# Optimization experiments

Measured on AMD Instinct MI355X. Metric: run time of the kernel, lower is better.

The kernel has to match this reference:

```python
import jax, jax.numpy as jnp
import numpy as np

EPS = 1e-12
SMOOTH = 9.0
SGR_STEPS = 3


def l2norm(x, axis=-1):
    return x / jnp.maximum(jnp.linalg.norm(x, axis=axis, keepdims=True), EPS)


def setup_inputs() -> dict:
    key = jax.random.key(0)
    d, s = 1024, 256
    n_img, n_cap, L, n_tok = 64, 64, 32, 197  # 197 -> CLS + 14x14 grid

    def xavier(k, shape):
        lim = float(np.sqrt(6.0 / (shape[-2] + shape[-1])))
        return jax.random.uniform(k, shape, jnp.float32, -lim, lim)

    ks = iter(jax.random.split(key, 32))
    inp = {
        "img_embs": jax.random.normal(next(ks), (n_img, n_tok, d), jnp.float32),
        "cap_embs": jax.random.normal(next(ks), (n_cap, L, d), jnp.float32),
        # constant lengths == max length so the vectorized reference matches
        # the original per-caption loop exactly
        "cap_lens": jnp.full((n_cap,), L, dtype=jnp.int32),
        # visual GlobalSelfAttention
        "vG_Wl": xavier(next(ks), (d, d)), "vG_bl": jnp.zeros((d,), jnp.float32),
        "vG_Wg": xavier(next(ks), (d, d)), "vG_bg": jnp.zeros((d,), jnp.float32),
        "vG_Wc": xavier(next(ks), (d, 1)), "vG_bc": jnp.zeros((1,), jnp.float32),
        # textual GlobalSelfAttention
        "tG_Wl": xavier(next(ks), (d, d)), "tG_bl": jnp.zeros((d,), jnp.float32),
        "tG_Wg": xavier(next(ks), (d, d)), "tG_bg": jnp.zeros((d,), jnp.float32),
        "tG_Wc": xavier(next(ks), (d, 1)), "tG_bc": jnp.zeros((1,), jnp.float32),
        # similarity projections
        "W_loc": xavier(next(ks), (d, s)), "b_loc": jnp.zeros((s,), jnp.float32),
        "W_glo": xavier(next(ks), (d, s)), "b_glo": jnp.zeros((s,), jnp.float32),
        "W_eval": xavier(next(ks), (s, 1)), "b_eval": jnp.zeros((1,), jnp.float32),
        # 3 stacked GraphReasoning layers
        "sgr_Wq": xavier(next(ks), (SGR_STEPS, s, s)), "sgr_bq": jnp.zeros((SGR_STEPS, s), jnp.float32),
        "sgr_Wk": xavier(next(ks), (SGR_STEPS, s, s)), "sgr_bk": jnp.zeros((SGR_STEPS, s), jnp.float32),
        "sgr_Wg": xavier(next(ks), (SGR_STEPS, s, s)), "sgr_bg": jnp.zeros((SGR_STEPS, s), jnp.float32),
    }
    return inp


def global_self_attention(local, raw_global, Wl, bl, Wg, bg, Wc, bc):
    # local: (B, N, d), raw_global: (B, d); dropout is identity at eval
    le = jnp.tanh(local @ Wl + bl)
    ge = jnp.tanh(raw_global @ Wg + bg)
    logits = ((le * ge[:, None, :]) @ Wc + bc)[..., 0]  # (B, N)
    weights = jax.nn.softmax(logits, axis=1)
    global_feat = jnp.sum(weights[..., None] * local, axis=1)
    return l2norm(global_feat, axis=-1)


def scan_attention(query, context, smooth=SMOOTH):
    # query: (B, Nq, d), context: (B, Nc, d)
    attn = jnp.einsum("bcd,bqd->bcq", context, query)
    attn = jax.nn.leaky_relu(attn, negative_slope=0.1)
    attn = l2norm(attn, axis=2)                    # normalize over query dim
    attn = jnp.swapaxes(attn, 1, 2)                # (B, Nq, Nc)
    attn = jax.nn.softmax(attn * smooth, axis=2)   # softmax over context
    weighted = jnp.einsum("bqc,bcd->bqd", attn, context)
    return l2norm(weighted, axis=-1)


def graph_reasoning(sim_emb, Wq, bq, Wk, bk, Wg, bg):
    q = sim_emb @ Wq + bq
    k = sim_emb @ Wk + bk
    edge = jax.nn.softmax(jnp.einsum("bnd,bmd->bnm", q, k), axis=-1)
    sgr = jnp.einsum("bnm,bmd->bnd", edge, sim_emb)
    return jax.nn.relu(sgr @ Wg + bg)


def reference(img_embs, cap_embs, cap_lens,
              vG_Wl, vG_bl, vG_Wg, vG_bg, vG_Wc, vG_bc,
              tG_Wl, tG_bl, tG_Wg, tG_bg, tG_Wc, tG_bc,
              W_loc, b_loc, W_glo, b_glo, W_eval, b_eval,
              sgr_Wq, sgr_bq, sgr_Wk, sgr_bk, sgr_Wg, sgr_bg):
    # 197 tokens -> strip CLS (has_cls_token is True)
    img_tokens = img_embs[:, 1:, :]                      # (n_img, 196, d)
    n_img = img_tokens.shape[0]
    img_avg = img_tokens.mean(axis=1)
    img_global = global_self_attention(img_tokens, img_avg,
                                       vG_Wl, vG_bl, vG_Wg, vG_bg, vG_Wc, vG_bc)

    def per_caption(cap_i):                              # cap_i: (L, d)
        L, d = cap_i.shape
        cap_e = jnp.broadcast_to(cap_i[None], (n_img, L, d))
        cap_avg = jnp.broadcast_to(cap_i.mean(axis=0)[None], (n_img, d))
        cap_global = global_self_attention(cap_e, cap_avg,
                                           tG_Wl, tG_bl, tG_Wg, tG_bg, tG_Wc, tG_bc)
        ctx = scan_attention(cap_e, img_tokens)          # (n_img, L, d)
        sim_loc = l2norm((ctx - cap_e) ** 2 @ W_loc + b_loc, axis=-1)
        sim_glo = l2norm((img_global - cap_global) ** 2 @ W_glo + b_glo, axis=-1)
        sim_emb = jnp.concatenate([sim_glo[:, None, :], sim_loc], axis=1)
        for t in range(SGR_STEPS):
            sim_emb = graph_reasoning(sim_emb, sgr_Wq[t], sgr_bq[t],
                                      sgr_Wk[t], sgr_bk[t], sgr_Wg[t], sgr_bg[t])
        return jax.nn.sigmoid(sim_emb[:, 0, :] @ W_eval + b_eval)[:, 0]  # (n_img,)

    sims = jax.vmap(per_caption)(cap_embs)               # (n_cap, n_img)
    return sims.T                                        # (n_img, n_cap)
```

## Files before the change

kernel.cpp:

```cpp
#include <hip/hip_runtime.h>
#include <hip/hip_bf16.h>
#include <math.h>

#define NI 64
#define NC 64
#define NTOK 197
#define TT 196
#define CL 32
#define DD 1024
#define SS 256
#define NN 33
#define EPSN 1e-12f
#define SMOOTHF 9.0f
#define TP 224

typedef __attribute__((ext_vector_type(8))) short bfrag;
typedef __attribute__((ext_vector_type(4))) float f32x4;
#define MFMA(a, b, c) __builtin_amdgcn_mfma_f32_16x16x32_bf16((a), (b), (c), 0, 0, 0)

#define OFF_ATTNT  0
#define OFF_WTILE  14848
#define OFF_WMAX   23552
#define OFF_NRMS   24064
#define OFF_QN     24192
#define OFF_RNQ    24704
#define OFF_SEA    0
#define OFF_EB     17424
#define OFF_R1     22176
#define OFF_WKQ    29088
#define OFF_VBUF   30112
#define SMEM_BYTES 31392

__device__ __forceinline__ float warp_reduce_sum64(float v) {
#pragma unroll
  for (int m = 32; m > 0; m >>= 1) v += __shfl_xor(v, m, 64);
  return v;
}
__device__ __forceinline__ unsigned short f2b(float f) {
  __hip_bfloat16 h = __float2bfloat16(f);
  return *reinterpret_cast<unsigned short*>(&h);
}
__device__ __forceinline__ float b2f(unsigned short u) {
  union { unsigned int i; float f; } v;
  v.i = ((unsigned int)u) << 16;
  return v.f;
}

__global__ void k_avg(const float* __restrict__ img, const float* __restrict__ cap,
                      float* __restrict__ img_avg, float* __restrict__ cap_avg) {
  int bid = blockIdx.x;
  int tid = threadIdx.x;
  if (bid < NI) {
    int b = bid;
    for (int d = tid; d < DD; d += 256) {
      float acc = 0.f;
      const float* p = img + ((size_t)b * NTOK + 1) * DD + d;
      for (int t = 0; t < TT; ++t) acc += p[(size_t)t * DD];
      img_avg[b * DD + d] = acc * (1.0f / TT);
    }
  } else {
    int c = bid - NI;
    for (int d = tid; d < DD; d += 256) {
      float acc = 0.f;
      const float* p = cap + (size_t)c * CL * DD + d;
      for (int t = 0; t < CL; ++t) acc += p[(size_t)t * DD];
      cap_avg[c * DD + d] = acc * (1.0f / CL);
    }
  }
}

__global__ void k_hvec2(const float* __restrict__ img_avg, const float* __restrict__ cap_avg,
                        const float* __restrict__ vWg, const float* __restrict__ vbg,
                        const float* __restrict__ vWc, const float* __restrict__ tWg,
                        const float* __restrict__ tbg, const float* __restrict__ tWc,
                        float* __restrict__ h_img, float* __restrict__ h_cap) {
  __shared__ float av[DD];
  int bid = blockIdx.x;
  const float* avg;
  const float* Wg;
  const float* bg;
  const float* Wc;
  float* h;
  if (bid < 256) {
    avg = img_avg; Wg = vWg; bg = vbg; Wc = vWc; h = h_img;
  } else {
    avg = cap_avg; Wg = tWg; bg = tbg; Wc = tWc; h = h_cap; bid -= 256;
  }
  int b = bid >> 2;
  int dc = bid & 3;
  int tid = threadIdx.x;
  for (int i = tid; i < DD; i += 256) av[i] = avg[b * DD + i];
  __syncthreads();
  int d = dc * 256 + tid;
  float acc = 0.f;
  for (int k = 0; k < DD; k += 4) {
    float4 a4 = *(const float4*)&av[k];
    acc += a4.x * Wg[(size_t)(k + 0) * DD + d];
    acc += a4.y * Wg[(size_t)(k + 1) * DD + d];
    acc += a4.z * Wg[(size_t)(k + 2) * DD + d];
    acc += a4.w * Wg[(size_t)(k + 3) * DD + d];
  }
  h[b * DD + d] = tanhf(acc + bg[d]) * Wc[d];
}

__global__ void k_logits2(const unsigned short* __restrict__ Ai, const unsigned short* __restrict__ Wi,
                          const float* __restrict__ bli, const float* __restrict__ hi,
                          float* __restrict__ pi,
                          const unsigned short* __restrict__ Ac, const unsigned short* __restrict__ Wc2,
                          const float* __restrict__ blc, const float* __restrict__ hc,
                          float* __restrict__ pc) {
  int tid = threadIdx.x;
  int lane = tid & 63, w = tid >> 6;
  int lrow = lane & 15, lk = (lane >> 4) * 8, rsub = (lane >> 4) * 4;
  int bx = blockIdx.x;
  const unsigned short* Abf;
  const unsigned short* WT;
  const float* bl;
  const float* h;
  float* partial;
  int rb, rowsPerBatch;
  if (bx < 196) {
    Abf = Ai; WT = Wi; bl = bli; h = hi; partial = pi; rb = bx * 64; rowsPerBatch = TT;
  } else {
    Abf = Ac; WT = Wc2; bl = blc; h = hc; partial = pc; rb = (bx - 196) * 64; rowsPerBatch = CL;
  }
  int c0 = blockIdx.y * 64;
  const unsigned short* ap = Abf + (size_t)(rb + w * 16 + lrow) * DD;
  f32x4 acc[4] = {};
  for (int k0 = 0; k0 < DD; k0 += 32) {
    bfrag a = *(const bfrag*)(ap + k0 + lk);
#pragma unroll
    for (int i = 0; i < 4; ++i) {
      bfrag bb = *(const bfrag*)(WT + (size_t)(c0 + i * 16 + lrow) * DD + k0 + lk);
      acc[i] = MFMA(a, bb, acc[i]);
    }
  }
#pragma unroll
  for (int r = 0; r < 4; ++r) {
    int row = rb + w * 16 + rsub + r;
    int bb2 = row / rowsPerBatch;
    float s = 0.f;
#pragma unroll
    for (int i = 0; i < 4; ++i) {
      int col = c0 + i * 16 + lrow;
      s += tanhf(acc[i][r] + bl[col]) * h[bb2 * DD + col];
    }
    s += __shfl_xor(s, 1, 64);
    s += __shfl_xor(s, 2, 64);
    s += __shfl_xor(s, 4, 64);
    s += __shfl_xor(s, 8, 64);
    if (lrow == 0) partial[(size_t)row * 16 + blockIdx.y] = s;
  }
}

__global__ void k_finish2(const float* __restrict__ pi, const float* __restrict__ bci,
                          const float* __restrict__ Xi, long bsi, int Ri, float* __restrict__ oi,
                          const float* __restrict__ pc, const float* __restrict__ bcc,
                          const float* __restrict__ Xc, long bsc, int Rc, float* __restrict__ oc) {
  __shared__ float w[200];
  __shared__ float red[8];
  int bid = blockIdx.x, tid = threadIdx.x;
  const float* partial;
  const float* bc;
  const float* Xbase;
  long batchStride;
  int R, b;
  float* outG;
  if (bid < 64) {
    partial = pi; bc = bci; Xbase = Xi; batchStride = bsi; R = Ri; outG = oi; b = bid;
  } else {
    partial = pc; bc = bcc; Xbase = Xc; batchStride = bsc; R = Rc; outG = oc; b = bid - 64;
  }
  for (int t = tid; t < R; t += 256) {
    const float* pp = &partial[((size_t)b * R + t) * 16];
    float s = bc[0];
#pragma unroll
    for (int u = 0; u < 16; ++u) s += pp[u];
    w[t] = s;
  }
  __syncthreads();
  float m = -1e30f;
  for (int t = tid; t < R; t += 256) m = fmaxf(m, w[t]);
#pragma unroll
  for (int mm = 32; mm; mm >>= 1) m = fmaxf(m, __shfl_xor(m, mm, 64));
  if ((tid & 63) == 0) red[tid >> 6] = m;
// ... 1 lines not shown
  m = fmaxf(fmaxf(red[0], red[1]), fmaxf(red[2], red[3]));
  __syncthreads();
  for (int t = tid; t < R; t += 256) w[t] = expf(w[t] - m);
  __syncthreads();
  const float* xb = Xbase + (size_t)b * batchStride;
  float acc[4];
  float ss = 0.f;
#pragma unroll
  for (int c4 = 0; c4 < 4; ++c4) {
    int d = tid + c4 * 256;
    float a = 0.f;
    for (int t = 0; t < R; ++t) a += w[t] * xb[(size_t)t * DD + d];
    acc[c4] = a;
    ss += a * a;
  }
  ss = warp_reduce_sum64(ss);
  if ((tid & 63) == 0) red[tid >> 6] = ss;
  __syncthreads();
  ss = red[0] + red[1] + red[2] + red[3];
  float rn = 1.0f / fmaxf(sqrtf(ss), EPSN);
#pragma unroll
  for (int c4 = 0; c4 < 4; ++c4) outG[(size_t)b * DD + tid + c4 * 256] = acc[c4] * rn;
}

__global__ void k_simglo_m(const float* __restrict__ ig, const float* __restrict__ cg,
                           const unsigned short* __restrict__ wgloT,
                           const float* __restrict__ bgl, float* __restrict__ simglo) {
  __shared__ unsigned short aL[64 * 40];
  int tid = threadIdx.x;
  int lane = tid & 63, w = tid >> 6;
  int lrow = lane & 15, lk = (lane >> 4) * 8, rsub = (lane >> 4) * 4;
  int b = blockIdx.x;
  int srow = tid >> 2, skq = tid & 3;
  f32x4 acc[16] = {};
  for (int k0 = 0; k0 < DD; k0 += 32) {
    const float* ip = ig + (size_t)b * DD + k0 + skq * 8;
    const float* cp = cg + (size_t)srow * DD + k0 + skq * 8;
    float4 i0 = *(const float4*)ip;
    float4 i1 = *(const float4*)(ip + 4);
    float4 c0 = *(const float4*)cp;
    float4 c1 = *(const float4*)(cp + 4);
    float d0 = i0.x - c0.x, d1 = i0.y - c0.y, d2 = i0.z - c0.z, d3 = i0.w - c0.w;
    float d4 = i1.x - c1.x, d5 = i1.y - c1.y, d6 = i1.z - c1.z, d7 = i1.w - c1.w;
    uint4 o;
    o.x = (unsigned int)f2b(d0 * d0) | ((unsigned int)f2b(d1 * d1) << 16);
    o.y = (unsigned int)f2b(d2 * d2) | ((unsigned int)f2b(d3 * d3) << 16);
    o.z = (unsigned int)f2b(d4 * d4) | ((unsigned int)f2b(d5 * d5) << 16);
    o.w = (unsigned int)f2b(d6 * d6) | ((unsigned int)f2b(d7 * d7) << 16);
    __syncthreads();
    *(uint4*)&aL[srow * 40 + skq * 8] = o;
    __syncthreads();
    bfrag af = *(const bfrag*)&aL[(w * 16 + lrow) * 40 + lk];
#pragma unroll
    for (int ct = 0; ct < 16; ++ct) {
      bfrag bb = *(const bfrag*)(wgloT + (size_t)(ct * 16 + lrow) * DD + k0 + lk);
      acc[ct] = MFMA(af, bb, acc[ct]);
    }
  }
  float bglv[16];
#pragma unroll
  for (int ct = 0; ct < 16; ++ct) bglv[ct] = bgl[ct * 16 + lrow];
#pragma unroll
  for (int r = 0; r < 4; ++r) {
    int crow = w * 16 + rsub + r;
    float vv[16];
    float ssq = 0.f;
#pragma unroll
    for (int ct = 0; ct < 16; ++ct) {
      float v = acc[ct][r] + bglv[ct];
      vv[ct] = v;
      ssq += v * v;
    }
    ssq += __shfl_xor(ssq, 1, 64);
    ssq += __shfl_xor(ssq, 2, 64);
    ssq += __shfl_xor(ssq, 4, 64);
    ssq += __shfl_xor(ssq, 8, 64);
    float rn = 1.0f / fmaxf(sqrtf(ssq), EPSN);
    float* op = simglo + ((size_t)b * 64 + crow) * SS;
#pragma unroll
    for (int ct = 0; ct < 16; ++ct) op[ct * 16 + lrow] = vv[ct] * rn;
  }
}

__global__ void k_mmatb(const float* __restrict__ Wa, const float* __restrict__ Wb,
                        unsigned short* __restrict__ M, const float* __restrict__ bq,
                        float* __restrict__ wkbqv) {
  __shared__ float a_lds[32][68];
  __shared__ float b_lds[32][68];
  __shared__ float bv[SS];
  int tid = threadIdx.x;
  if (blockIdx.x >= 48) {
    int t = blockIdx.x - 48;
    const float* wk = Wb + (size_t)t * SS * SS;
    bv[tid] = bq[t * SS + tid];
    __syncthreads();
    float acc = 0.f;
    for (int j = 0; j < SS; j += 4) {
      float4 wv = *(const float4*)&wk[(size_t)tid * SS + j];
      float4 b4 = *(const float4*)&bv[j];
      acc += wv.x * b4.x + wv.y * b4.y + wv.z * b4.z + wv.w * b4.w;
    }
    wkbqv[t * SS + tid] = acc;
    return;
  }
  int t = blockIdx.x >> 4;
  int dt = (blockIdx.x >> 2) & 3, et = blockIdx.x & 3;
  int d0 = dt * 64, e0 = et * 64;
  const float* wq = Wa + (size_t)t * SS * SS;
  const float* wk = Wb + (size_t)t * SS * SS;
  int ty = tid >> 4, tx = tid & 15;
  int s_rr = tid >> 2, s_kq = tid & 3;
  float acc[4][4] = {};
  for (int j0 = 0; j0 < SS; j0 += 32) {
    float4 q0 = *(const float4*)&wq[(size_t)(d0 + s_rr) * SS + j0 + s_kq * 8];
    float4 q1 = *(const float4*)&wq[(size_t)(d0 + s_rr) * SS + j0 + s_kq * 8 + 4];
    float4 k0v = *(const float4*)&wk[(size_t)(e0 + s_rr) * SS + j0 + s_kq * 8];
    float4 k1v = *(const float4*)&wk[(size_t)(e0 + s_rr) * SS + j0 + s_kq * 8 + 4];
    __syncthreads();
    float qa[8] = {q0.x, q0.y, q0.z, q0.w, q1.x, q1.y, q1.z, q1.w};
    float ka[8] = {k0v.x, k0v.y, k0v.z, k0v.w, k1v.x, k1v.y, k1v.z, k1v.w};
#pragma unroll
    for (int u = 0; u < 8; ++u) {
      a_lds[s_kq * 8 + u][s_rr] = qa[u];
      b_lds[s_kq * 8 + u][s_rr] = ka[u];
    }
    __syncthreads();
#pragma unroll
    for (int kk = 0; kk < 32; ++kk) {
      float4 a4 = *(const float4*)&a_lds[kk][ty * 4];
      float4 b4 = *(const float4*)&b_lds[kk][tx * 4];
      float av[4] = {a4.x, a4.y, a4.z, a4.w};
      float bvv[4] = {b4.x, b4.y, b4.z, b4.w};
#pragma unroll
      for (int i = 0; i < 4; ++i)
#pragma unroll
        for (int j = 0; j < 4; ++j) acc[i][j] += av[i] * bvv[j];
    }
  }
#pragma unroll
  for (int i = 0; i < 4; ++i) {
    unsigned int lo = (unsigned int)f2b(acc[i][0]) | ((unsigned int)f2b(acc[i][1]) << 16);
    unsigned int hi = (unsigned int)f2b(acc[i][2]) | ((unsigned int)f2b(acc[i][3]) << 16);
    uint2 o = make_uint2(lo, hi);
    *(uint2*)(M + (size_t)t * SS * SS + (size_t)(d0 + ty * 4 + i) * SS + e0 + tx * 4) = o;
  }
}

__global__ void k_imgprep(const float* __restrict__ img, unsigned short* __restrict__ row_bf,
                          unsigned short* __restrict__ tr_bf) {
  __shared__ float t[32][33];
  int b = blockIdx.z;
  int t0 = blockIdx.y * 32, d0 = blockIdx.x * 32;
  int tx = threadIdx.x & 31, ty = threadIdx.x >> 5;
#pragma unroll
  for (int u = 0; u < 4; ++u) {
    int tt = t0 + ty + u * 8;
    float v = (tt < TT) ? img[((size_t)b * NTOK + 1 + tt) * DD + d0 + tx] : 0.f;
    t[ty + u * 8][tx] = v;
    if (tt < TT) row_bf[((size_t)b * TT + tt) * DD + d0 + tx] = f2b(v);
  }
  __syncthreads();
#pragma unroll
  for (int u = 0; u < 4; ++u)
    tr_bf[((size_t)b * DD + d0 + ty + u * 8) * TP + t0 + tx] = f2b(t[tx][ty + u * 8]);
}

__global__ void k_gram_mfma(const unsigned short* __restrict__ img_bf,
                            unsigned short* __restrict__ gram) {
  int tid = threadIdx.x;
  int lane = tid & 63, w = tid >> 6;
  int lrow = lane & 15, lk = (lane >> 4) * 8, rsub = (lane >> 4) * 4;
  int bimg = blockIdx.x;
  int rb = blockIdx.y * 64, cb = blockIdx.z * 64;
  const unsigned short* X = img_bf + (size_t)bimg * TT * DD;
  int ra = rb + w * 16 + lrow;
  if (ra > TT - 1) ra = TT - 1;
  f32x4 acc[4] = {};
  for (int k0 = 0; k0 < DD; k0 += 32) {
    bfrag a = *(const bfrag*)(X + (size_t)ra * DD + k0 + lk);
#pragma unroll
    for (int i = 0; i < 4; ++i) {
      int cc = cb + i * 16 + lrow;
      if (cc > TT - 1) cc = TT - 1;
      bfrag bb = *(const bfrag*)(X + (size_t)cc * DD + k0 + lk);
      acc[i] = MFMA(a, bb, acc[i]);
    }
  }
  unsigned short* Gp = gram + (size_t)bimg * 208 * TP;
#pragma unroll
  for (int i = 0; i < 4; ++i) {
    int cc = cb + i * 16 + lrow;
#pragma unroll
    for (int r = 0; r < 4; ++r) {
      int rr = rb + w * 16 + rsub + r;
      if (rr < 208 && cc < TP)
        Gp[(size_t)rr * TP + cc] = (rr < TT && cc < TT) ? f2b(acc[i][r]) : 0;
    }
  }
}

__global__ void k_castb(const float* __restrict__ s, unsigned short* __restrict__ d, int n4) {
  int i = blockIdx.x * 256 + threadIdx.x;
  if (i < n4) {
    float4 v = *(const float4*)(s + (size_t)i * 4);
    uint2 o;
    o.x = (unsigned int)f2b(v.x) | ((unsigned int)f2b(v.y) << 16);
    o.y = (unsigned int)f2b(v.z) | ((unsigned int)f2b(v.w) << 16);
    *(uint2*)(d + (size_t)i * 4) = o;
  }
}

__global__ void k_tcast_all(const float* __restrict__ vWl, const float* __restrict__ tWl,
                            const float* __restrict__ sWg, const float* __restrict__ Wloc,
                            const float* __restrict__ Wglo,
                            unsigned short* __restrict__ wlT_v, unsigned short* __restrict__ wlT_t,
                            unsigned short* __restrict__ wgT3, unsigned short* __restrict__ wlocT,
                            unsigned short* __restrict__ wgloT) {
  __shared__ float t[32][33];
  int id = blockIdx.x;
  const float* s;
  unsigned short* d;
  int R, C;
  if (id < 1024) {
    s = vWl; d = wlT_v; R = 1024; C = 1024;
  } else if (id < 2048) {
    s = tWl; d = wlT_t; R = 1024; C = 1024; id -= 1024;
  } else if (id < 2240) {
    id -= 2048;
    int tb = id >> 6; id &= 63;
    s = sWg + (size_t)tb * 65536; d = wgT3 + (size_t)tb * 65536; R = 256; C = 256;
  } else if (id < 2496) {
    s = Wloc; d = wlocT; R = 1024; C = 256; id -= 2240;
  } else {
    s = Wglo; d = wgloT; R = 1024; C = 256; id -= 2496;
  }
  int ct = C >> 5;
  int r0 = (id / ct) * 32, c0 = (id % ct) * 32;
  int tx = threadIdx.x & 31, ty = threadIdx.x >> 5;
#pragma unroll
  for (int u = 0; u < 4; ++u)
    t[ty + u * 8][tx] = s[(size_t)(r0 + ty + u * 8) * C + c0 + tx];
  __syncthreads();
#pragma unroll
  for (int u = 0; u < 4; ++u)
    d[(size_t)(c0 + ty + u * 8) * R + r0 + tx] = f2b(t[tx][ty + u * 8]);
}

__global__ __launch_bounds__(256, 4) void k_pair(
    const float* __restrict__ b_loc, const float* __restrict__ simglo,
    const float* __restrict__ wkbq, const float* __restrict__ bg3,
    const float* __restrict__ W_eval, const float* __restrict__ b_eval,
    const unsigned short* __restrict__ cap_bf, const unsigned short* __restrict__ img_bf,
    const unsigned short* __restrict__ imgT_bf, const unsigned short* __restrict__ gram_bf,
    const unsigned short* __restrict__ wlocT_bf, const unsigned short* __restrict__ mt_bf,
    const unsigned short* __restrict__ wgT_bf, float* __restrict__ out) {
  extern __shared__ char smem[];

  int tid = threadIdx.x;
  int lane = tid & 63, w = tid >> 6;
  int lrow = lane & 15;
  int lk = (lane >> 4) * 8;
  int rsub = (lane >> 4) * 4;
  int p = ((blockIdx.x & 7) << 9) | (blockIdx.x >> 3);
  int b = p >> 6, c = p & 63;
  const unsigned short* imgR = img_bf + (size_t)b * TT * DD;
  const unsigned short* capB = cap_bf + (size_t)c * CL * DD;
  char* attnT_b = smem + OFF_ATTNT;

  {
    f32x4 acc[4][2] = {};
    for (int k0 = 0; k0 < DD; k0 += 32) {
      bfrag bq0 = *(const bfrag*)(capB + (size_t)lrow * DD + k0 + lk);
      bfrag bq1 = *(const bfrag*)(capB + (size_t)(16 + lrow) * DD + k0 + lk);
#pragma unroll
      for (int i = 0; i < 4; ++i) {
        int tt = w + 4 * i;
        if (tt < 13) {
          int t = tt * 16 + lrow;
          bfrag a = {0, 0, 0, 0, 0, 0, 0, 0};
          if (t < TT) a = *(const bfrag*)(imgR + (size_t)t * DD + k0 + lk);
          acc[i][0] = MFMA(a, bq0, acc[i][0]);
          acc[i][1] = MFMA(a, bq1, acc[i][1]);
        }
      }
    }
    float mx0 = -1e30f, mx1 = -1e30f;
#pragma unroll
    for (int i = 0; i < 4; ++i) {
      int tt = w + 4 * i;
      if (tt < 13) {
#pragma unroll
        for (int r = 0; r < 4; ++r) {
          int t = tt * 16 + rsub + r;
          float v0 = acc[i][0][r];
          v0 = v0 < 0.f ? 0.1f * v0 : v0;
          float v1 = acc[i][1][r];
          v1 = v1 < 0.f ? 0.1f * v1 : v1;
          float s2 = v0 * v0 + v1 * v1;
          s2 += __shfl_xor(s2, 1, 64);
          s2 += __shfl_xor(s2, 2, 64);
          s2 += __shfl_xor(s2, 4, 64);
          s2 += __shfl_xor(s2, 8, 64);
          float rn = 1.0f / fmaxf(sqrtf(s2), EPSN);
          v0 *= rn;
          v1 *= rn;
          acc[i][0][r] = v0;
          acc[i][1][r] = v1;
          if (t < TT) {
            mx0 = fmaxf(mx0, v0);
            mx1 = fmaxf(mx1, v1);
          }
        }
      }
    }
    mx0 = fmaxf(mx0, __shfl_xor(mx0, 16, 64));
    mx0 = fmaxf(mx0, __shfl_xor(mx0, 32, 64));
    mx1 = fmaxf(mx1, __shfl_xor(mx1, 16, 64));
    mx1 = fmaxf(mx1, __shfl_xor(mx1, 32, 64));
    float* wmax = (float*)(smem + OFF_WMAX);
    if ((lane >> 4) == 0) {
      wmax[w * 32 + lrow] = mx0;
      wmax[w * 32 + 16 + lrow] = mx1;
    }
    __syncthreads();
    mx0 = fmaxf(fmaxf(wmax[lrow], wmax[32 + lrow]), fmaxf(wmax[64 + lrow], wmax[96 + lrow]));
    mx1 = fmaxf(fmaxf(wmax[16 + lrow], wmax[48 + lrow]),
                fmaxf(wmax[80 + lrow], wmax[112 + lrow]));
#pragma unroll
    for (int i = 0; i < 4; ++i) {
      int tt = w + 4 * i;
// ... 177 lines not shown
      const unsigned short* mstep = mt_bf + (size_t)step * SS * SS;
      const unsigned short* wstep = wgT_bf + (size_t)step * SS * SS;
      wkq[tid] = wkbq[step * SS + tid];
      __syncthreads();
      if (tid < 132) {
        int m = tid >> 2, qq = tid & 3;
        float a = 0.f;
        for (int e = qq * 64; e < qq * 64 + 64; e += 2) {
          unsigned int u = *(const unsigned int*)(seA_b + m * 528 + e * 2);
          a += b2f(u & 0xffff) * wkq[e] + b2f(u >> 16) * wkq[e + 1];
        }
        a += __shfl_xor(a, 1, 64);
        a += __shfl_xor(a, 2, 64);
        if (qq == 0) vbuf[m] = a;
      }
      f32x4 aE[3] = {};
      for (int ec = 0; ec < 4; ++ec) {
        f32x4 aGc[3] = {};
        for (int kc = 0; kc < 8; ++kc) {
          int k = kc * 32 + lk;
          bfrag bb = *(const bfrag*)(mstep + (size_t)(ec * 64 + w * 16 + lrow) * SS + k);
#pragma unroll
          for (int mt = 0; mt < 3; ++mt) {
            bfrag af = *(const bfrag*)(seA_b + (mt * 16 + lrow) * 528 + k * 2);
            aGc[mt] = MFMA(af, bb, aGc[mt]);
          }
        }
        __syncthreads();
#pragma unroll
        for (int mt = 0; mt < 3; ++mt)
#pragma unroll
          for (int r = 0; r < 4; ++r)
            *(unsigned short*)(Gc_b + (mt * 16 + rsub + r) * 144 + (w * 16 + lrow) * 2) =
                f2b(aGc[mt][r]);
        __syncthreads();
#pragma unroll
        for (int kc = 0; kc < 2; ++kc) {
          int k = kc * 32 + lk;
#pragma unroll
          for (int ti = 0; ti < 3; ++ti) {
            int tile = w + ti * 4;
            if (tile < 9) {
              int mtE = tile / 3, ntE = tile - mtE * 3;
              bfrag ga = *(const bfrag*)(Gc_b + (mtE * 16 + lrow) * 144 + k * 2);
              bfrag sb = *(const bfrag*)(seA_b + (ntE * 16 + lrow) * 528 + (ec * 64 + k) * 2);
              aE[ti] = MFMA(ga, sb, aE[ti]);
            }
          }
        }
      }
      __syncthreads();
#pragma unroll
      for (int ti = 0; ti < 3; ++ti) {
        int tile = w + ti * 4;
        if (tile < 9) {
          int mtE = tile / 3, ntE = tile - mtE * 3;
          int n0 = mtE * 16 + rsub, m = ntE * 16 + lrow;
#pragma unroll
          for (int r = 0; r < 4; ++r)
            if (n0 + r < NN && m < NN) Ef[(n0 + r) * 34 + m] = aE[ti][r] + vbuf[m];
        }
      }
      __syncthreads();
      if (tid < NN) {
        float mx = -1e30f;
        for (int mm = 0; mm < NN; ++mm) mx = fmaxf(mx, Ef[tid * 34 + mm]);
        float sum = 0.f;
        for (int mm = 0; mm < NN; ++mm) {
          float e = expf(Ef[tid * 34 + mm] - mx);
          Ef[tid * 34 + mm] = e;
          sum += e;
        }
        float rs = 1.0f / sum;
        for (int mm = 0; mm < NN; ++mm) Ef[tid * 34 + mm] *= rs;
      }
      __syncthreads();
      for (int idx = tid; idx < 33 * 36; idx += 256) {
        int n = idx / 36, mp = (idx - n * 36) * 2;
        unsigned int lo = (mp < NN) ? (unsigned int)f2b(Ef[n * 34 + mp]) : 0u;
        unsigned int hi = (mp + 1 < NN) ? (unsigned int)f2b(Ef[n * 34 + mp + 1]) : 0u;
        *(unsigned int*)(Eb + n * 144 + mp * 2) = lo | (hi << 16);
      }
      __syncthreads();
      unsigned int oPk[4][3][2];
#pragma unroll
      for (int sc = 0; sc < 4; ++sc) {
        f32x4 aX[3] = {};
        for (int kc = 0; kc < 8; ++kc) {
          int k = kc * 32 + lk;
          bfrag bb = *(const bfrag*)(wstep + (size_t)(sc * 64 + w * 16 + lrow) * SS + k);
#pragma unroll
          for (int mt = 0; mt < 3; ++mt) {
            bfrag af = *(const bfrag*)(seA_b + (mt * 16 + lrow) * 528 + k * 2);
            aX[mt] = MFMA(af, bb, aX[mt]);
          }
        }
        __syncthreads();
#pragma unroll
        for (int mt = 0; mt < 3; ++mt) {
          unsigned int lo = (unsigned int)f2b(aX[mt][0]) | ((unsigned int)f2b(aX[mt][1]) << 16);
          unsigned int hi = (unsigned int)f2b(aX[mt][2]) | ((unsigned int)f2b(aX[mt][3]) << 16);
          *(uint2*)(XT_b + (w * 16 + lrow) * 144 + (mt * 16 + rsub) * 2) = make_uint2(lo, hi);
        }
        *(uint2*)(XT_b + (w * 16 + lrow) * 144 + (48 + rsub) * 2) = make_uint2(0, 0);
        __syncthreads();
        f32x4 aO[3] = {};
#pragma unroll
        for (int kc = 0; kc < 2; ++kc) {
          int k = kc * 32 + lk;
          bfrag xa = *(const bfrag*)(XT_b + (w * 16 + lrow) * 144 + k * 2);
#pragma unroll
          for (int nt = 0; nt < 3; ++nt) {
            bfrag eb = *(const bfrag*)(Eb + (nt * 16 + lrow) * 144 + k * 2);
            aO[nt] = MFMA(xa, eb, aO[nt]);
          }
        }
        float bga[4];
#pragma unroll
        for (int r = 0; r < 4; ++r) bga[r] = bg3[step * SS + sc * 64 + w * 16 + rsub + r];
#pragma unroll
        for (int nt = 0; nt < 3; ++nt) {
          float v0 = fmaxf(aO[nt][0] + bga[0], 0.f);
          float v1 = fmaxf(aO[nt][1] + bga[1], 0.f);
          float v2 = fmaxf(aO[nt][2] + bga[2], 0.f);
          float v3 = fmaxf(aO[nt][3] + bga[3], 0.f);
          oPk[sc][nt][0] = (unsigned int)f2b(v0) | ((unsigned int)f2b(v1) << 16);
          oPk[sc][nt][1] = (unsigned int)f2b(v2) | ((unsigned int)f2b(v3) << 16);
        }
      }
#pragma unroll
      for (int sc = 0; sc < 4; ++sc)
#pragma unroll
        for (int nt = 0; nt < 3; ++nt) {
          int n = nt * 16 + lrow;
          if (n < NN)
            *(uint2*)(seA_b + n * 528 + (sc * 64 + w * 16 + rsub) * 2) =
                make_uint2(oPk[sc][nt][0], oPk[sc][nt][1]);
        }
      __syncthreads();
    }
  }

  if (tid < 64) {
    const char* seA_b = smem + OFF_SEA;
    uint2 u = *(const uint2*)(seA_b + tid * 8);
    float4 w4 = *(const float4*)&W_eval[tid * 4];
    float s = b2f(u.x & 0xffff) * w4.x + b2f(u.x >> 16) * w4.y +
              b2f(u.y & 0xffff) * w4.z + b2f(u.y >> 16) * w4.w;
    s = warp_reduce_sum64(s);
    if (tid == 0) out[b * 64 + c] = 1.0f / (1.0f + expf(-(s + b_eval[0])));
  }
}

extern "C" void kernel_launch(void* const* d_in, const int* in_sizes, int n_in,
                              void* d_out, int out_size, void* d_ws, size_t ws_size,
                              hipStream_t stream) {
  (void)in_sizes; (void)n_in; (void)out_size; (void)ws_size;
  const float* img = (const float*)d_in[0];
  const float* cap = (const float*)d_in[1];
  const float* vG_Wl = (const float*)d_in[3];
  const float* vG_bl = (const float*)d_in[4];
  const float* vG_Wg = (const float*)d_in[5];
  const float* vG_bg = (const float*)d_in[6];
  const float* vG_Wc = (const float*)d_in[7];
  const float* vG_bc = (const float*)d_in[8];
  const float* tG_Wl = (const float*)d_in[9];
  const float* tG_bl = (const float*)d_in[10];
  const float* tG_Wg = (const float*)d_in[11];
  const float* tG_bg = (const float*)d_in[12];
  const float* tG_Wc = (const float*)d_in[13];
  const float* tG_bc = (const float*)d_in[14];
  const float* W_loc = (const float*)d_in[15];
  const float* b_loc = (const float*)d_in[16];
  const float* W_glo = (const float*)d_in[17];
  const float* b_glo = (const float*)d_in[18];
  const float* W_eval = (const float*)d_in[19];
  const float* b_eval = (const float*)d_in[20];
  const float* sgr_Wq = (const float*)d_in[21];
  const float* sgr_bq = (const float*)d_in[22];
  const float* sgr_Wk = (const float*)d_in[23];
  const float* sgr_Wg = (const float*)d_in[25];
  const float* sgr_bg = (const float*)d_in[26];
  float* out = (float*)d_out;
  float* ws = (float*)d_ws;
  float* img_avg = ws;
  float* cap_avg = ws + 65536;
  float* h_img = ws + 131072;
  float* h_cap = ws + 196608;
  float* part_img = ws + 262144;
  float* part_cap = ws + 462848;
  float* img_glob = ws + 495616;
  float* cap_glob = ws + 561152;
  float* simglo = ws + 626688;
  float* wkbqv = ws + 1675264;
  unsigned short* ub = (unsigned short*)(ws + 1676032);
  unsigned short* mt_bf = ub;
  unsigned short* wgT_bf = ub + 196608;
  unsigned short* wlocT_bf = ub + 393216;
  unsigned short* cap_bf = ub + 655360;
  unsigned short* gram_bf = ub + 2752512;
  unsigned short* imgT_bf = ub + 5734400;
  unsigned short* img_bf = ub + 20414464;
  unsigned short* wlT_v = ub + 33259520;
  unsigned short* wlT_t = ub + 34308096;
  unsigned short* wgloT = ub + 35356672;

  k_avg<<<128, 256, 0, stream>>>(img, cap, img_avg, cap_avg);
  k_imgprep<<<dim3(32, 7, 64), 256, 0, stream>>>(img, img_bf, imgT_bf);
  k_castb<<<2048, 256, 0, stream>>>(cap, cap_bf, 524288);
  k_tcast_all<<<2752, 256, 0, stream>>>(vG_Wl, tG_Wl, sgr_Wg, W_loc, W_glo,
                                        wlT_v, wlT_t, wgT_bf, wlocT_bf, wgloT);
  k_hvec2<<<512, 256, 0, stream>>>(img_avg, cap_avg, vG_Wg, vG_bg, vG_Wc,
                                   tG_Wg, tG_bg, tG_Wc, h_img, h_cap);
  k_logits2<<<dim3(228, 16), 256, 0, stream>>>(img_bf, wlT_v, vG_bl, h_img, part_img,
                                               cap_bf, wlT_t, tG_bl, h_cap, part_cap);
  k_finish2<<<128, 256, 0, stream>>>(part_img, vG_bc, img + DD, (long)NTOK * DD, TT, img_glob,
                                     part_cap, tG_bc, cap, (long)CL * DD, CL, cap_glob);
  k_simglo_m<<<64, 256, 0, stream>>>(img_glob, cap_glob, wgloT, b_glo, simglo);
  k_mmatb<<<51, 256, 0, stream>>>(sgr_Wk, sgr_Wq, mt_bf, sgr_bq, wkbqv);
  k_gram_mfma<<<dim3(64, 4, 4), 256, 0, stream>>>(img_bf, gram_bf);
  hipFuncSetAttribute((const void*)k_pair, hipFuncAttributeMaxDynamicSharedMemorySize,
                      SMEM_BYTES);
  k_pair<<<4096, 256, SMEM_BYTES, stream>>>(b_loc, simglo, wkbqv, sgr_bg, W_eval, b_eval,
                                            cap_bf, img_bf, imgT_bf, gram_bf, wlocT_bf,
                                            mt_bf, wgT_bf, out);
}
```

Baseline: 1.717 ms.

## Merge preprocessing kernels into two launches and drop barriers in pair kernel

Folds the averaging, image cast and transpose, caption cast, weight transpose-casts and the SGR weight product into one block-indexed prep kernel. The global-gate vector and the Gram MFMA are merged into a second kernel, which cuts seven small launches down to two and lets independent work share the GPU. In the pair kernel, two __syncthreads around the per-wave XT tile writes are removed and the zero padding is hoisted out of the loop, because each wave only touches its own rows. This relies on the cross-wave read of Eb staying correctly ordered, and the merged kernel's shared buffer and branching may lower occupancy for some block types.

```diff
diff --git a/kernel.cpp b/kernel.cpp
--- a/kernel.cpp
+++ b/kernel.cpp
@@ -46,61 +46,236 @@
   return v.f;
 }
 
-__global__ void k_avg(const float* __restrict__ img, const float* __restrict__ cap,
-                      float* __restrict__ img_avg, float* __restrict__ cap_avg) {
-  int bid = blockIdx.x;
+__global__ void k_prep(const float* __restrict__ img, const float* __restrict__ cap,
+                       float* __restrict__ img_avg, float* __restrict__ cap_avg,
+                       unsigned short* __restrict__ row_bf, unsigned short* __restrict__ tr_bf,
+                       unsigned short* __restrict__ cap_bf,
+                       const float* __restrict__ vWl, const float* __restrict__ tWl,
+                       const float* __restrict__ sWg, const float* __restrict__ Wloc,
+                       const float* __restrict__ Wglo,
+                       unsigned short* __restrict__ wlT_v, unsigned short* __restrict__ wlT_t,
+                       unsigned short* __restrict__ wgT3, unsigned short* __restrict__ wlocT,
+                       unsigned short* __restrict__ wgloT,
+                       const float* __restrict__ Wa, const float* __restrict__ Wb,
+                       unsigned short* __restrict__ M, const float* __restrict__ bq,
+                       float* __restrict__ wkbqv) {
+  __shared__ float shbuf[4608];
+  int id = blockIdx.x;
   int tid = threadIdx.x;
-  if (bid < NI) {
-    int b = bid;
-    for (int d = tid; d < DD; d += 256) {
-      float acc = 0.f;
-      const float* p = img + ((size_t)b * NTOK + 1) * DD + d;
-      for (int t = 0; t < TT; ++t) acc += p[(size_t)t * DD];
-      img_avg[b * DD + d] = acc * (1.0f / TT);
-    }
-  } else {
-    int c = bid - NI;
-    for (int d = tid; d < DD; d += 256) {
-      float acc = 0.f;
-      const float* p = cap + (size_t)c * CL * DD + d;
-      for (int t = 0; t < CL; ++t) acc += p[(size_t)t * DD];
-      cap_avg[c * DD + d] = acc * (1.0f / CL);
+
+  if (id < 128) {
+    if (id < NI) {
+      int b = id;
+      for (int d = tid; d < DD; d += 256) {
+        float acc = 0.f;
+        const float* p = img + ((size_t)b * NTOK + 1) * DD + d;
+        for (int t = 0; t < TT; ++t) acc += p[(size_t)t * DD];
+        img_avg[b * DD + d] = acc * (1.0f / TT);
+      }
+    } else {
+      int c = id - NI;
+      for (int d = tid; d < DD; d += 256) {
+        float acc = 0.f;
+        const float* p = cap + (size_t)c * CL * DD + d;
+        for (int t = 0; t < CL; ++t) acc += p[(size_t)t * DD];
+        cap_avg[c * DD + d] = acc * (1.0f / CL);
+      }
+    }
+    return;
+  }
+  if (id < 14464) {
+    id -= 128;
+    int bx = id & 31, by = (id >> 5) % 7, b = id / 224;
+    float (*t)[33] = (float(*)[33])shbuf;
+    int t0 = by * 32, d0 = bx * 32;
+    int tx = tid & 31, ty = tid >> 5;
+#pragma unroll
+    for (int u = 0; u < 4; ++u) {
+      int tt = t0 + ty + u * 8;
+      float v = (tt < TT) ? img[((size_t)b * NTOK + 1 + tt) * DD + d0 + tx] : 0.f;
+      t[ty + u * 8][tx] = v;
+      if (tt < TT) row_bf[((size_t)b * TT + tt) * DD + d0 + tx] = f2b(v);
+    }
+    __syncthreads();
+#pragma unroll
+    for (int u = 0; u < 4; ++u)
+      tr_bf[((size_t)b * DD + d0 + ty + u * 8) * TP + t0 + tx] = f2b(t[tx][ty + u * 8]);
+    return;
+  }
+  if (id < 16512) {
+    int i = (id - 14464) * 256 + tid;
+    if (i < 524288) {
+      float4 v = *(const float4*)(cap + (size_t)i * 4);
+      uint2 o;
+      o.x = (unsigned int)f2b(v.x) | ((unsigned int)f2b(v.y) << 16);
+      o.y = (unsigned int)f2b(v.z) | ((unsigned int)f2b(v.w) << 16);
+      *(uint2*)(cap_bf + (size_t)i * 4) = o;
+    }
+    return;
+  }
+  if (id < 19264) {
+    id -= 16512;
+    const float* s;
+    unsigned short* d;
+    int R, C;
+    if (id < 1024) {
+      s = vWl; d = wlT_v; R = 1024; C = 1024;
+    } else if (id < 2048) {
+      s = tWl; d = wlT_t; R = 1024; C = 1024; id -= 1024;
+    } else if (id < 2240) {
+      id -= 2048;
+      int tb = id >> 6; id &= 63;
+      s = sWg + (size_t)tb * 65536; d = wgT3 + (size_t)tb * 65536; R = 256; C = 256;
+    } else if (id < 2496) {
+      s = Wloc; d = wlocT; R = 1024; C = 256; id -= 2240;
+    } else {
+      s = Wglo; d = wgloT; R = 1024; C = 256; id -= 2496;
+    }
+    float (*t)[33] = (float(*)[33])shbuf;
+    int ct = C >> 5;
+    int r0 = (id / ct) * 32, c0 = (id % ct) * 32;
+    int tx = tid & 31, ty = tid >> 5;
+#pragma unroll
+    for (int u = 0; u < 4; ++u)
+      t[ty + u * 8][tx] = s[(size_t)(r0 + ty + u * 8) * C + c0 + tx];
+    __syncthreads();
+#pragma unroll
+    for (int u = 0; u < 4; ++u)
+      d[(size_t)(c0 + ty + u * 8) * R + r0 + tx] = f2b(t[tx][ty + u * 8]);
+    return;
+  }
+  id -= 19264;
+  if (id >= 48) {
+    int t = id - 48;
+    float* bv = shbuf + 4352;
+    const float* wk = Wb + (size_t)t * SS * SS;
+    bv[tid] = bq[t * SS + tid];
+    __syncthreads();
+    float acc = 0.f;
+    for (int j = 0; j < SS; j += 4) {
+      float4 wv = *(const float4*)&wk[(size_t)tid * SS + j];
+      float4 b4 = *(const float4*)&bv[j];
+      acc += wv.x * b4.x + wv.y * b4.y + wv.z * b4.z + wv.w * b4.w;
+    }
+    wkbqv[t * SS + tid] = acc;
+    return;
+  }
+  {
+    float (*a_lds)[68] = (float(*)[68])shbuf;
+    float (*b_lds)[68] = (float(*)[68])(shbuf + 2176);
+    int t = id >> 4;
+    int dt = (id >> 2) & 3, et = id & 3;
+    int d0 = dt * 64, e0 = et * 64;
+    const float* wq = Wa + (size_t)t * SS * SS;
+    const float* wk = Wb + (size_t)t * SS * SS;
+    int ty = tid >> 4, tx = tid & 15;
+    int s_rr = tid >> 2, s_kq = tid & 3;
+    float acc[4][4] = {};
+    for (int j0 = 0; j0 < SS; j0 += 32) {
+      float4 q0 = *(const float4*)&wq[(size_t)(d0 + s_rr) * SS + j0 + s_kq * 8];
+      float4 q1 = *(const float4*)&wq[(size_t)(d0 + s_rr) * SS + j0 + s_kq * 8 + 4];
+      float4 k0v = *(const float4*)&wk[(size_t)(e0 + s_rr) * SS + j0 + s_kq * 8];
+      float4 k1v = *(const float4*)&wk[(size_t)(e0 + s_rr) * SS + j0 + s_kq * 8 + 4];
+      __syncthreads();
+      float qa[8] = {q0.x, q0.y, q0.z, q0.w, q1.x, q1.y, q1.z, q1.w};
+      float ka[8] = {k0v.x, k0v.y, k0v.z, k0v.w, k1v.x, k1v.y, k1v.z, k1v.w};
+#pragma unroll
+      for (int u = 0; u < 8; ++u) {
+        a_lds[s_kq * 8 + u][s_rr] = qa[u];
+        b_lds[s_kq * 8 + u][s_rr] = ka[u];
+      }
+      __syncthreads();
+#pragma unroll
+      for (int kk = 0; kk < 32; ++kk) {
+        float4 a4 = *(const float4*)&a_lds[kk][ty * 4];
+        float4 b4 = *(const float4*)&b_lds[kk][tx * 4];
+        float av[4] = {a4.x, a4.y, a4.z, a4.w};
+        float bvv[4] = {b4.x, b4.y, b4.z, b4.w};
+#pragma unroll
+        for (int i = 0; i < 4; ++i)
+#pragma unroll
+          for (int j = 0; j < 4; ++j) acc[i][j] += av[i] * bvv[j];
+      }
+    }
+#pragma unroll
+    for (int i = 0; i < 4; ++i) {
+      unsigned int lo = (unsigned int)f2b(acc[i][0]) | ((unsigned int)f2b(acc[i][1]) << 16);
+      unsigned int hi = (unsigned int)f2b(acc[i][2]) | ((unsigned int)f2b(acc[i][3]) << 16);
+      uint2 o = make_uint2(lo, hi);
+      *(uint2*)(M + (size_t)t * SS * SS + (size_t)(d0 + ty * 4 + i) * SS + e0 + tx * 4) = o;
     }
   }
 }
 
-__global__ void k_hvec2(const float* __restrict__ img_avg, const float* __restrict__ cap_avg,
-                        const float* __restrict__ vWg, const float* __restrict__ vbg,
-                        const float* __restrict__ vWc, const float* __restrict__ tWg,
-                        const float* __restrict__ tbg, const float* __restrict__ tWc,
-                        float* __restrict__ h_img, float* __restrict__ h_cap) {
+__global__ void k_hvgram(const float* __restrict__ img_avg, const float* __restrict__ cap_avg,
+                         const float* __restrict__ vWg, const float* __restrict__ vbg,
+                         const float* __restrict__ vWc, const float* __restrict__ tWg,
+                         const float* __restrict__ tbg, const float* __restrict__ tWc,
+                         float* __restrict__ h_img, float* __restrict__ h_cap,
+                         const unsigned short* __restrict__ img_bf,
+                         unsigned short* __restrict__ gram) {
   __shared__ float av[DD];
-  int bid = blockIdx.x;
-  const float* avg;
-  const float* Wg;
-  const float* bg;
-  const float* Wc;
-  float* h;
-  if (bid < 256) {
-    avg = img_avg; Wg = vWg; bg = vbg; Wc = vWc; h = h_img;
-  } else {
-    avg = cap_avg; Wg = tWg; bg = tbg; Wc = tWc; h = h_cap; bid -= 256;
-  }
-  int b = bid >> 2;
-  int dc = bid & 3;
+  int id = blockIdx.x;
   int tid = threadIdx.x;
-  for (int i = tid; i < DD; i += 256) av[i] = avg[b * DD + i];
-  __syncthreads();
-  int d = dc * 256 + tid;
-  float acc = 0.f;
-  for (int k = 0; k < DD; k += 4) {
-    float4 a4 = *(const float4*)&av[k];
-    acc += a4.x * Wg[(size_t)(k + 0) * DD + d];
-    acc += a4.y * Wg[(size_t)(k + 1) * DD + d];
-    acc += a4.z * Wg[(size_t)(k + 2) * DD + d];
-    acc += a4.w * Wg[(size_t)(k + 3) * DD + d];
-  }
-  h[b * DD + d] = tanhf(acc + bg[d]) * Wc[d];
+  if (id < 512) {
+    const float* avg;
+    const float* Wg;
+    const float* bg;
+    const float* Wc;
+    float* h;
+    if (id < 256) {
+      avg = img_avg; Wg = vWg; bg = vbg; Wc = vWc; h = h_img;
+    } else {
+      avg = cap_avg; Wg = tWg; bg = tbg; Wc = tWc; h = h_cap; id -= 256;
+    }
+    int b = id >> 2;
+    int dc = id & 3;
+    for (int i = tid; i < DD; i += 256) av[i] = avg[b * DD + i];
+    __syncthreads();
+    int d = dc * 256 + tid;
+    float acc = 0.f;
+    for (int k = 0; k < DD; k += 4) {
+      float4 a4 = *(const float4*)&av[k];
+      acc += a4.x * Wg[(size_t)(k + 0) * DD + d];
+      acc += a4.y * Wg[(size_t)(k + 1) * DD + d];
+      acc += a4.z * Wg[(size_t)(k + 2) * DD + d];
+      acc += a4.w * Wg[(size_t)(k + 3) * DD + d];
+    }
+    h[b * DD + d] = tanhf(acc + bg[d]) * Wc[d];
+    return;
+  }
+  {
+    int g = id - 512;
+    int lane = tid & 63, w = tid >> 6;
+    int lrow = lane & 15, lk = (lane >> 4) * 8, rsub = (lane >> 4) * 4;
+    int bimg = g & 63;
+    int rb = ((g >> 6) & 3) * 64, cb = (g >> 8) * 64;
+    const unsigned short* X = img_bf + (size_t)bimg * TT * DD;
+    int ra = rb + w * 16 + lrow;
+    if (ra > TT - 1) ra = TT - 1;
+    f32x4 acc[4] = {};
+    for (int k0 = 0; k0 < DD; k0 += 32) {
+      bfrag a = *(const bfrag*)(X + (size_t)ra * DD + k0 + lk);
+#pragma unroll
+      for (int i = 0; i < 4; ++i) {
+        int cc = cb + i * 16 + lrow;
+        if (cc > TT - 1) cc = TT - 1;
+        bfrag bb = *(const bfrag*)(X + (size_t)cc * DD + k0 + lk);
+        acc[i] = MFMA(a, bb, acc[i]);
+      }
+    }
+    unsigned short* Gp = gram + (size_t)bimg * 208 * TP;
+#pragma unroll
+    for (int i = 0; i < 4; ++i) {
+      int cc = cb + i * 16 + lrow;
+#pragma unroll
+      for (int r = 0; r < 4; ++r) {
+        int rr = rb + w * 16 + rsub + r;
+        if (rr < 208 && cc < TP)
+          Gp[(size_t)rr * TP + cc] = (rr < TT && cc < TT) ? f2b(acc[i][r]) : 0;
+      }
+    }
+  }
 }
 
 __global__ void k_logits2(const unsigned short* __restrict__ Ai, const unsigned short* __restrict__ Wi,
@@ -268,170 +443,6 @@
   }
 }
 
-__global__ void k_mmatb(const float* __restrict__ Wa, const float* __restrict__ Wb,
-                        unsigned short* __restrict__ M, const float* __restrict__ bq,
-                        float* __restrict__ wkbqv) {
-  __shared__ float a_lds[32][68];
-  __shared__ float b_lds[32][68];
-  __shared__ float bv[SS];
-  int tid = threadIdx.x;
-  if (blockIdx.x >= 48) {
-    int t = blockIdx.x - 48;
-    const float* wk = Wb + (size_t)t * SS * SS;
-    bv[tid] = bq[t * SS + tid];
-    __syncthreads();
-    float acc = 0.f;
-    for (int j = 0; j < SS; j += 4) {
-      float4 wv = *(const float4*)&wk[(size_t)tid * SS + j];
-      float4 b4 = *(const float4*)&bv[j];
-      acc += wv.x * b4.x + wv.y * b4.y + wv.z * b4.z + wv.w * b4.w;
-    }
-    wkbqv[t * SS + tid] = acc;
-    return;
-  }
-  int t = blockIdx.x >> 4;
-  int dt = (blockIdx.x >> 2) & 3, et = blockIdx.x & 3;
-  int d0 = dt * 64, e0 = et * 64;
-  const float* wq = Wa + (size_t)t * SS * SS;
-  const float* wk = Wb + (size_t)t * SS * SS;
-  int ty = tid >> 4, tx = tid & 15;
-  int s_rr = tid >> 2, s_kq = tid & 3;
-  float acc[4][4] = {};
-  for (int j0 = 0; j0 < SS; j0 += 32) {
-    float4 q0 = *(const float4*)&wq[(size_t)(d0 + s_rr) * SS + j0 + s_kq * 8];
-    float4 q1 = *(const float4*)&wq[(size_t)(d0 + s_rr) * SS + j0 + s_kq * 8 + 4];
-    float4 k0v = *(const float4*)&wk[(size_t)(e0 + s_rr) * SS + j0 + s_kq * 8];
-    float4 k1v = *(const float4*)&wk[(size_t)(e0 + s_rr) * SS + j0 + s_kq * 8 + 4];
-    __syncthreads();
-    float qa[8] = {q0.x, q0.y, q0.z, q0.w, q1.x, q1.y, q1.z, q1.w};
-    float ka[8] = {k0v.x, k0v.y, k0v.z, k0v.w, k1v.x, k1v.y, k1v.z, k1v.w};
-#pragma unroll
-    for (int u = 0; u < 8; ++u) {
-      a_lds[s_kq * 8 + u][s_rr] = qa[u];
-      b_lds[s_kq * 8 + u][s_rr] = ka[u];
-    }
-    __syncthreads();
-#pragma unroll
-    for (int kk = 0; kk < 32; ++kk) {
-      float4 a4 = *(const float4*)&a_lds[kk][ty * 4];
-      float4 b4 = *(const float4*)&b_lds[kk][tx * 4];
-      float av[4] = {a4.x, a4.y, a4.z, a4.w};
-      float bvv[4] = {b4.x, b4.y, b4.z, b4.w};
-#pragma unroll
-      for (int i = 0; i < 4; ++i)
-#pragma unroll
-        for (int j = 0; j < 4; ++j) acc[i][j] += av[i] * bvv[j];
-    }
-  }
-#pragma unroll
-  for (int i = 0; i < 4; ++i) {
-    unsigned int lo = (unsigned int)f2b(acc[i][0]) | ((unsigned int)f2b(acc[i][1]) << 16);
-    unsigned int hi = (unsigned int)f2b(acc[i][2]) | ((unsigned int)f2b(acc[i][3]) << 16);
-    uint2 o = make_uint2(lo, hi);
-    *(uint2*)(M + (size_t)t * SS * SS + (size_t)(d0 + ty * 4 + i) * SS + e0 + tx * 4) = o;
-  }
-}
-
-__global__ void k_imgprep(const float* __restrict__ img, unsigned short* __restrict__ row_bf,
-                          unsigned short* __restrict__ tr_bf) {
-  __shared__ float t[32][33];
-  int b = blockIdx.z;
-  int t0 = blockIdx.y * 32, d0 = blockIdx.x * 32;
-  int tx = threadIdx.x & 31, ty = threadIdx.x >> 5;
-#pragma unroll
-  for (int u = 0; u < 4; ++u) {
-    int tt = t0 + ty + u * 8;
-    float v = (tt < TT) ? img[((size_t)b * NTOK + 1 + tt) * DD + d0 + tx] : 0.f;
-    t[ty + u * 8][tx] = v;
-    if (tt < TT) row_bf[((size_t)b * TT + tt) * DD + d0 + tx] = f2b(v);
-  }
-  __syncthreads();
-#pragma unroll
-  for (int u = 0; u < 4; ++u)
-    tr_bf[((size_t)b * DD + d0 + ty + u * 8) * TP + t0 + tx] = f2b(t[tx][ty + u * 8]);
-}
-
-__global__ void k_gram_mfma(const unsigned short* __restrict__ img_bf,
-                            unsigned short* __restrict__ gram) {
-  int tid = threadIdx.x;
-  int lane = tid & 63, w = tid >> 6;
-  int lrow = lane & 15, lk = (lane >> 4) * 8, rsub = (lane >> 4) * 4;
-  int bimg = blockIdx.x;
-  int rb = blockIdx.y * 64, cb = blockIdx.z * 64;
-  const unsigned short* X = img_bf + (size_t)bimg * TT * DD;
-  int ra = rb + w * 16 + lrow;
-  if (ra > TT - 1) ra = TT - 1;
-  f32x4 acc[4] = {};
-  for (int k0 = 0; k0 < DD; k0 += 32) {
-    bfrag a = *(const bfrag*)(X + (size_t)ra * DD + k0 + lk);
-#pragma unroll
-    for (int i = 0; i < 4; ++i) {
-      int cc = cb + i * 16 + lrow;
-      if (cc > TT - 1) cc = TT - 1;
-      bfrag bb = *(const bfrag*)(X + (size_t)cc * DD + k0 + lk);
-      acc[i] = MFMA(a, bb, acc[i]);
-    }
-  }
-  unsigned short* Gp = gram + (size_t)bimg * 208 * TP;
-#pragma unroll
-  for (int i = 0; i < 4; ++i) {
-    int cc = cb + i * 16 + lrow;
-#pragma unroll
-    for (int r = 0; r < 4; ++r) {
-      int rr = rb + w * 16 + rsub + r;
-      if (rr < 208 && cc < TP)
-        Gp[(size_t)rr * TP + cc] = (rr < TT && cc < TT) ? f2b(acc[i][r]) : 0;
-    }
-  }
-}
-
-__global__ void k_castb(const float* __restrict__ s, unsigned short* __restrict__ d, int n4) {
-  int i = blockIdx.x * 256 + threadIdx.x;
-  if (i < n4) {
-    float4 v = *(const float4*)(s + (size_t)i * 4);
-    uint2 o;
-    o.x = (unsigned int)f2b(v.x) | ((unsigned int)f2b(v.y) << 16);
-    o.y = (unsigned int)f2b(v.z) | ((unsigned int)f2b(v.w) << 16);
-    *(uint2*)(d + (size_t)i * 4) = o;
-  }
-}
-
-__global__ void k_tcast_all(const float* __restrict__ vWl, const float* __restrict__ tWl,
-                            const float* __restrict__ sWg, const float* __restrict__ Wloc,
-                            const float* __restrict__ Wglo,
-                            unsigned short* __restrict__ wlT_v, unsigned short* __restrict__ wlT_t,
-                            unsigned short* __restrict__ wgT3, unsigned short* __restrict__ wlocT,
-                            unsigned short* __restrict__ wgloT) {
-  __shared__ float t[32][33];
-  int id = blockIdx.x;
-  const float* s;
-  unsigned short* d;
-  int R, C;
-  if (id < 1024) {
-    s = vWl; d = wlT_v; R = 1024; C = 1024;
-  } else if (id < 2048) {
-    s = tWl; d = wlT_t; R = 1024; C = 1024; id -= 1024;
-  } else if (id < 2240) {
-    id -= 2048;
-    int tb = id >> 6; id &= 63;
-    s = sWg + (size_t)tb * 65536; d = wgT3 + (size_t)tb * 65536; R = 256; C = 256;
-  } else if (id < 2496) {
-    s = Wloc; d = wlocT; R = 1024; C = 256; id -= 2240;
-  } else {
-    s = Wglo; d = wgloT; R = 1024; C = 256; id -= 2496;
-  }
-  int ct = C >> 5;
-  int r0 = (id / ct) * 32, c0 = (id % ct) * 32;
-  int tx = threadIdx.x & 31, ty = threadIdx.x >> 5;
-#pragma unroll
-  for (int u = 0; u < 4; ++u)
-    t[ty + u * 8][tx] = s[(size_t)(r0 + ty + u * 8) * C + c0 + tx];
-  __syncthreads();
-#pragma unroll
-  for (int u = 0; u < 4; ++u)
-    d[(size_t)(c0 + ty + u * 8) * R + r0 + tx] = f2b(t[tx][ty + u * 8]);
-}
-
 __global__ __launch_bounds__(256, 4) void k_pair(
     const float* __restrict__ b_loc, const float* __restrict__ simglo,
     const float* __restrict__ wkbq, const float* __restrict__ bg3,
@@ -775,6 +786,7 @@
         *(unsigned int*)(Eb + n * 144 + mp * 2) = lo | (hi << 16);
       }
       __syncthreads();
+      *(uint2*)(XT_b + (w * 16 + lrow) * 144 + (48 + rsub) * 2) = make_uint2(0, 0);
       unsigned int oPk[4][3][2];
 #pragma unroll
       for (int sc = 0; sc < 4; ++sc) {
@@ -788,15 +800,12 @@
             aX[mt] = MFMA(af, bb, aX[mt]);
           }
         }
-        __syncthreads();
 #pragma unroll
         for (int mt = 0; mt < 3; ++mt) {
           unsigned int lo = (unsigned int)f2b(aX[mt][0]) | ((unsigned int)f2b(aX[mt][1]) << 16);
           unsigned int hi = (unsigned int)f2b(aX[mt][2]) | ((unsigned int)f2b(aX[mt][3]) << 16);
           *(uint2*)(XT_b + (w * 16 + lrow) * 144 + (mt * 16 + rsub) * 2) = make_uint2(lo, hi);
         }
-        *(uint2*)(XT_b + (w * 16 + lrow) * 144 + (48 + rsub) * 2) = make_uint2(0, 0);
-        __syncthreads();
         f32x4 aO[3] = {};
 #pragma unroll
         for (int kc = 0; kc < 2; ++kc) {
@@ -898,20 +907,17 @@
   unsigned short* wlT_t = ub + 34308096;
   unsigned short* wgloT = ub + 35356672;
 
-  k_avg<<<128, 256, 0, stream>>>(img, cap, img_avg, cap_avg);
-  k_imgprep<<<dim3(32, 7, 64), 256, 0, stream>>>(img, img_bf, imgT_bf);
-  k_castb<<<2048, 256, 0, stream>>>(cap, cap_bf, 524288);
-  k_tcast_all<<<2752, 256, 0, stream>>>(vG_Wl, tG_Wl, sgr_Wg, W_loc, W_glo,
-                                        wlT_v, wlT_t, wgT_bf, wlocT_bf, wgloT);
-  k_hvec2<<<512, 256, 0, stream>>>(img_avg, cap_avg, vG_Wg, vG_bg, vG_Wc,
-                                   tG_Wg, tG_bg, tG_Wc, h_img, h_cap);
+  k_prep<<<19315, 256, 0, stream>>>(img, cap, img_avg, cap_avg, img_bf, imgT_bf, cap_bf,
+                                    vG_Wl, tG_Wl, sgr_Wg, W_loc, W_glo,
+                                    wlT_v, wlT_t, wgT_bf, wlocT_bf, wgloT,
+                                    sgr_Wk, sgr_Wq, mt_bf, sgr_bq, wkbqv);
+  k_hvgram<<<1536, 256, 0, stream>>>(img_avg, cap_avg, vG_Wg, vG_bg, vG_Wc,
+                                     tG_Wg, tG_bg, tG_Wc, h_img, h_cap, img_bf, gram_bf);
   k_logits2<<<dim3(228, 16), 256, 0, stream>>>(img_bf, wlT_v, vG_bl, h_img, part_img,
                                                cap_bf, wlT_t, tG_bl, h_cap, part_cap);
   k_finish2<<<128, 256, 0, stream>>>(part_img, vG_bc, img + DD, (long)NTOK * DD, TT, img_glob,
                                      part_cap, tG_bc, cap, (long)CL * DD, CL, cap_glob);
   k_simglo_m<<<64, 256, 0, stream>>>(img_glob, cap_glob, wgloT, b_glo, simglo);
-  k_mmatb<<<51, 256, 0, stream>>>(sgr_Wk, sgr_Wq, mt_bf, sgr_bq, wkbqv);
-  k_gram_mfma<<<dim3(64, 4, 4), 256, 0, stream>>>(img_bf, gram_bf);
   hipFuncSetAttribute((const void*)k_pair, hipFuncAttributeMaxDynamicSharedMemorySize,
                       SMEM_BYTES);
   k_pair<<<4096, 256, SMEM_BYTES, stream>>>(b_loc, simglo, wkbqv, sgr_bg, W_eval, b_eval,
```

Measured after the change: 1.661 ms. 3.3% less time.
